# Performance work log

Hardware: AMD Instinct MI355X
Metric: run time of the kernel (lower is better)

The kernel has to match this reference:

```python
import jax, jax.numpy as jnp
import numpy as np

DIM = 512; HEADS = 8; DH = 64; M = 256; ITERS = 6; N_PATCH = 10000; N_CLASSES = 2


def layernorm(x, w, b, eps=1e-5):
    mu = x.mean(-1, keepdims=True)
    var = ((x - mu) ** 2).mean(-1, keepdims=True)
    return (x - mu) * jax.lax.rsqrt(var + eps) * w + b


def pinv_iter(x, iters=ITERS):
    # Moore-Penrose iterative pseudo-inverse (lucidrains nystrom-attention)
    abs_x = jnp.abs(x)
    col = abs_x.sum(-1)
    row = abs_x.sum(-2)
    z = jnp.swapaxes(x, -1, -2) / (jnp.max(col) * jnp.max(row))
    I = jnp.eye(x.shape[-1], dtype=x.dtype)
    for _ in range(iters):
        xz = x @ z
        z = 0.25 * z @ (13 * I - xz @ (15 * I - xz @ (7 * I - xz)))
    return z


def nystrom_attn(x, qkv_w, out_w, out_b, res_w):
    b, n, _ = x.shape
    pad = (-n) % M  # front-pad so n divisible by num_landmarks
    xp = jnp.pad(x, ((0, 0), (pad, 0), (0, 0)))
    npad = n + pad
    qkv = (xp @ qkv_w).reshape(b, npad, 3, HEADS, DH)
    q = jnp.transpose(qkv[:, :, 0], (0, 2, 1, 3)) * (DH ** -0.5)  # [b,h,n,d]
    k = jnp.transpose(qkv[:, :, 1], (0, 2, 1, 3))
    v = jnp.transpose(qkv[:, :, 2], (0, 2, 1, 3))
    l = npad // M
    q_l = q.reshape(b, HEADS, M, l, DH).mean(3)  # landmark means [b,h,m,d]
    k_l = k.reshape(b, HEADS, M, l, DH).mean(3)
    attn1 = jax.nn.softmax(jnp.einsum('bhnd,bhmd->bhnm', q, k_l), -1)
    attn2 = jax.nn.softmax(jnp.einsum('bhid,bhjd->bhij', q_l, k_l), -1)
    attn3 = jax.nn.softmax(jnp.einsum('bhmd,bhnd->bhmn', q_l, k), -1)
    out = (attn1 @ pinv_iter(attn2)) @ (attn3 @ v)  # [b,h,n,d]
    pk = (res_w.shape[2] - 1) // 2
    out = out + jax.lax.conv_general_dilated(
        v, res_w, (1, 1), [(pk, pk), (0, 0)], feature_group_count=HEADS)
    out = jnp.transpose(out, (0, 2, 1, 3)).reshape(b, npad, HEADS * DH)
    out = out @ out_w + out_b
    return out[:, -n:]


def ppeg(x, H, W, w7, b7, w5, b5, w3, b3):
    B, _, C = x.shape
    cls_tok, feat = x[:, :1], x[:, 1:]
    f = jnp.transpose(feat, (0, 2, 1)).reshape(B, C, H, W)
    def dw(w, b):
        p = w.shape[2] // 2
        return jax.lax.conv_general_dilated(
            f, w, (1, 1), [(p, p), (p, p)], feature_group_count=C) + b[None, :, None, None]
    y = f + dw(w7, b7) + dw(w5, b5) + dw(w3, b3)
    y = jnp.transpose(y.reshape(B, C, H * W), (0, 2, 1))
    return jnp.concatenate([cls_tok, y], axis=1)


def setup_inputs() -> dict:
    key = jax.random.key(0)
    ks = jax.random.split(key, 16)
    d = {
        'x': jax.random.normal(ks[0], (1, N_PATCH, DIM), jnp.float32),
        'cls_token': jax.random.normal(ks[1], (1, 1, DIM), jnp.float32) * 1e-6,
        'ln1_w': jnp.ones((DIM,), jnp.float32), 'ln1_b': jnp.zeros((DIM,), jnp.float32),
        'qkv1_w': jax.random.normal(ks[2], (DIM, 3 * DIM), jnp.float32) * 0.03,
        'out1_w': jax.random.normal(ks[3], (DIM, DIM), jnp.float32) * 0.04,
        'out1_b': jnp.zeros((DIM,), jnp.float32),
        'res1_w': jax.random.normal(ks[4], (HEADS, 1, 33, 1), jnp.float32) * 0.1,
        'p7_w': jax.random.normal(ks[5], (DIM, 1, 7, 7), jnp.float32) * 0.1,
        'p7_b': jnp.zeros((DIM,), jnp.float32),
        'p5_w': jax.random.normal(ks[6], (DIM, 1, 5, 5), jnp.float32) * 0.1,
        'p5_b': jnp.zeros((DIM,), jnp.float32),
        'p3_w': jax.random.normal(ks[7], (DIM, 1, 3, 3), jnp.float32) * 0.1,
        'p3_b': jnp.zeros((DIM,), jnp.float32),
        'ln2_w': jnp.ones((DIM,), jnp.float32), 'ln2_b': jnp.zeros((DIM,), jnp.float32),
        'qkv2_w': jax.random.normal(ks[8], (DIM, 3 * DIM), jnp.float32) * 0.03,
        'out2_w': jax.random.normal(ks[9], (DIM, DIM), jnp.float32) * 0.04,
        'out2_b': jnp.zeros((DIM,), jnp.float32),
        'res2_w': jax.random.normal(ks[10], (HEADS, 1, 33, 1), jnp.float32) * 0.1,
        'norm_w': jnp.ones((DIM,), jnp.float32), 'norm_b': jnp.zeros((DIM,), jnp.float32),
        'fc2_w': jax.random.normal(ks[11], (DIM, N_CLASSES), jnp.float32) * 0.06,
        'fc2_b': jnp.zeros((N_CLASSES,), jnp.float32),
        'pc_w': jax.random.normal(ks[12], (DIM, N_CLASSES), jnp.float32) * 0.06,
        'pc_b': jnp.zeros((N_CLASSES,), jnp.float32),
    }
    return d


def reference(x, cls_token, ln1_w, ln1_b, qkv1_w, out1_w, out1_b, res1_w,
              p7_w, p7_b, p5_w, p5_b, p3_w, p3_b,
              ln2_w, ln2_b, qkv2_w, out2_w, out2_b, res2_w,
              norm_w, norm_b, fc2_w, fc2_b, pc_w, pc_b):
    h = x.astype(jnp.float32)
    B, n0, C = h.shape
    _H = int(np.ceil(np.sqrt(n0))); _W = _H
    add = _H * _W - n0
    if add > 0:
        h = jnp.concatenate([h, h[:, :add]], axis=1)
    h = jnp.concatenate([jnp.broadcast_to(cls_token, (B, 1, C)), h], axis=1)
    h = h + nystrom_attn(layernorm(h, ln1_w, ln1_b), qkv1_w, out1_w, out1_b, res1_w)
    h = ppeg(h, _H, _W, p7_w, p7_b, p5_w, p5_b, p3_w, p3_b)
    h = h + nystrom_attn(layernorm(h, ln2_w, ln2_b), qkv2_w, out2_w, out2_b, res2_w)
    hn = layernorm(h, norm_w, norm_b)
    cls_f = hn[:, 0]
    patch_f = hn[:, 1:]
    if add > 0:
        patch_f = patch_f[:, :n0]
    bag_logits = cls_f @ fc2_w + fc2_b
    patch_logits = patch_f @ pc_w + pc_b
    patch_scores = jax.nn.softmax(patch_logits, -1)
    return bag_logits, patch_logits, patch_scores
```

## Files before the change

### kernel.cpp

```cpp
#include <hip/hip_runtime.h>
#include <hip/hip_bf16.h>

#define DIM    512
#define HEADS  8
#define DHD    64
#define MLAND  256
#define NTOK   10001
#define NPATCH 10000
#define NPAD   10240
#define PADR   239
#define LFAC   40
#define MOUT   10112
#define NSPLIT 8

typedef __bf16 bf16x8_t __attribute__((ext_vector_type(8)));
typedef float  f32x4_t  __attribute__((ext_vector_type(4)));
typedef short  short8_t __attribute__((ext_vector_type(8)));

__device__ inline bf16x8_t bzero8() {
    union { short8_t s; bf16x8_t b; } u;
    u.s = (short8_t){0, 0, 0, 0, 0, 0, 0, 0};
    return u.b;
}

#define GLDS(gp, lp) __builtin_amdgcn_global_load_lds( \
    (const __attribute__((address_space(1))) void*)(gp), \
    (__attribute__((address_space(3))) void*)(lp), 16, 0, 0)

__global__ void k_concat(const float* __restrict__ x, const float* __restrict__ cls,
                         float* __restrict__ h) {
    int idx = blockIdx.x * 256 + threadIdx.x;
    if (idx >= NTOK * DIM) return;
    int row = idx / DIM, col = idx % DIM;
    h[idx] = (row == 0) ? cls[col] : x[(row - 1) * DIM + col];
}

__global__ void k_layernorm_bf(const float* __restrict__ h, const float* __restrict__ w,
                               const float* __restrict__ b, __hip_bfloat16* __restrict__ xbf) {
    int row = blockIdx.x;
    const float* r = h + (long)row * DIM;
    int t = threadIdx.x;
    float v0 = r[t], v1 = r[t + 256];
    __shared__ float red[256];
    red[t] = v0 + v1; __syncthreads();
    for (int o = 128; o > 0; o >>= 1) { if (t < o) red[t] += red[t + o]; __syncthreads(); }
    float mu = red[0] * (1.f / DIM); __syncthreads();
    float d0 = v0 - mu, d1 = v1 - mu;
    red[t] = d0 * d0 + d1 * d1; __syncthreads();
    for (int o = 128; o > 0; o >>= 1) { if (t < o) red[t] += red[t + o]; __syncthreads(); }
    float rstd = rsqrtf(red[0] * (1.f / DIM) + 1e-5f);
    long base = (long)(PADR + row) * DIM;
    xbf[base + t]       = __float2bfloat16(d0 * rstd * w[t] + b[t]);
    xbf[base + t + 256] = __float2bfloat16(d1 * rstd * w[t + 256] + b[t + 256]);
}

__global__ void k_zerobf(__hip_bfloat16* __restrict__ p, int n) {
    int i = blockIdx.x * 256 + threadIdx.x;
    if (i < n) p[i] = __float2bfloat16(0.f);
}
__global__ void k_wt_cvt(const float* __restrict__ W, __hip_bfloat16* __restrict__ Wt,
                         int K, int N) {
    __shared__ float tile[32][33];
    int k0 = blockIdx.x * 32, n0 = blockIdx.y * 32;
    int lx = threadIdx.x % 32, ly = threadIdx.x / 32;
    for (int i = 0; i < 32; i += 8) tile[ly + i][lx] = W[(long)(k0 + ly + i) * N + n0 + lx];
    __syncthreads();
    for (int i = 0; i < 32; i += 8)
        Wt[(long)(n0 + ly + i) * K + k0 + lx] = __float2bfloat16(tile[lx][ly + i]);
}
__global__ void k_vt(const __hip_bfloat16* __restrict__ vh, __hip_bfloat16* __restrict__ vt) {
    __shared__ __hip_bfloat16 tile[32][33];
    int n0 = blockIdx.x * 32, d0 = blockIdx.y * 32, h = blockIdx.z;
    int lx = threadIdx.x % 32, ly = threadIdx.x / 32;
    for (int i = 0; i < 32; i += 8)
        tile[ly + i][lx] = vh[((long)h * NPAD + n0 + ly + i) * 64 + d0 + lx];
    __syncthreads();
    for (int i = 0; i < 32; i += 8)
        vt[((long)h * 64 + d0 + ly + i) * NPAD + n0 + lx] = tile[lx][ly + i];
}

__global__ __launch_bounds__(256) void k_qkv_gemm(
    const __hip_bfloat16* __restrict__ A, const __hip_bfloat16* __restrict__ Bt,
    __hip_bfloat16* __restrict__ qh, __hip_bfloat16* __restrict__ kh,
    __hip_bfloat16* __restrict__ vh)
{
    const int K = 512;
    __shared__ unsigned short As[128 * 64];
    __shared__ unsigned short Bs[128 * 64];
    int tid = threadIdx.x;
    int m0 = blockIdx.y * 128, n0 = blockIdx.x * 128;
    int wave = tid >> 6, lane = tid & 63;
    int wm = (wave & 1) * 64, wn = (wave >> 1) * 64;
    f32x4_t zero4 = {0.f, 0.f, 0.f, 0.f};
    f32x4_t acc[4][4];
#pragma unroll
    for (int i = 0; i < 4; i++)
#pragma unroll
        for (int j = 0; j < 4; j++) acc[i][j] = zero4;
    int quad = lane >> 4, fr = lane & 15;
    int lrow8 = lane >> 3, gls = lane & 7;
    int gg = gls ^ lrow8;

    for (int k0 = 0; k0 < K; k0 += 64) {
        __syncthreads();
#pragma unroll
        for (int rnd = 0; rnd < 4; rnd++) {
            int r0 = rnd * 32 + wave * 8;
            int ar = r0 + lrow8;
            GLDS(A  + (long)(m0 + ar) * K + k0 + gg * 8, &As[r0 * 64]);
            GLDS(Bt + (long)(n0 + ar) * K + k0 + gg * 8, &Bs[r0 * 64]);
        }
        __syncthreads();
#pragma unroll
        for (int ks = 0; ks < 2; ks++) {
            int sg = (ks * 4 + quad) ^ (fr & 7);
            bf16x8_t af[4], bq[4];
#pragma unroll
            for (int i = 0; i < 4; i++) {
                af[i] = *(const bf16x8_t*)&As[(wm + i * 16 + fr) * 64 + sg * 8];
                bq[i] = *(const bf16x8_t*)&Bs[(wn + i * 16 + fr) * 64 + sg * 8];
            }
#pragma unroll
            for (int i = 0; i < 4; i++)
#pragma unroll
                for (int j = 0; j < 4; j++)
                    acc[i][j] = __builtin_amdgcn_mfma_f32_16x16x32_bf16(af[i], bq[j], acc[i][j], 0, 0, 0);
        }
    }
    int col = lane & 15, rq = lane >> 4;
#pragma unroll
    for (int j = 0; j < 4; j++) {
        int c = n0 + wn + j * 16 + col;
        int sect = c >> 9;
        int hh = (c >> 6) & 7;
        int d = c & 63;
        __hip_bfloat16* dst = (sect == 0) ? qh : (sect == 1) ? kh : vh;
        float sc = (sect == 0) ? 0.125f : 1.f;
#pragma unroll
        for (int i = 0; i < 4; i++) {
            int rbase = m0 + wm + i * 16 + rq * 4;
#pragma unroll
            for (int rr = 0; rr < 4; rr++) {
                int r = rbase + rr;
                dst[((long)hh * NPAD + r) * 64 + d] = __float2bfloat16(acc[i][j][rr] * sc);
            }
        }
    }
}

__global__ __launch_bounds__(256) void k_mfma_gemm(
    const __hip_bfloat16* __restrict__ A, const __hip_bfloat16* __restrict__ Bt,
    float* __restrict__ C, int M, int N, int K, int Mstore,
    const float* __restrict__ bias, int accum)
{
    __shared__ unsigned short As[128 * 64];
    __shared__ unsigned short Bs[128 * 64];
    int tid = threadIdx.x;
    int m0 = blockIdx.y * 128, n0 = blockIdx.x * 128;
    int wave = tid >> 6, lane = tid & 63;
    int wm = (wave & 1) * 64, wn = (wave >> 1) * 64;
    f32x4_t zero4 = {0.f, 0.f, 0.f, 0.f};
    f32x4_t acc[4][4];
#pragma unroll
    for (int i = 0; i < 4; i++)
#pragma unroll
        for (int j = 0; j < 4; j++) acc[i][j] = zero4;
    int quad = lane >> 4, fr = lane & 15;
    int lrow8 = lane >> 3, gls = lane & 7;
    int gg = gls ^ lrow8;

    for (int k0 = 0; k0 < K; k0 += 64) {
        __syncthreads();
#pragma unroll
        for (int rnd = 0; rnd < 4; rnd++) {
            int r0 = rnd * 32 + wave * 8;
            int ar = r0 + lrow8;
            GLDS(A  + (long)(m0 + ar) * K + k0 + gg * 8, &As[r0 * 64]);
            GLDS(Bt + (long)(n0 + ar) * K + k0 + gg * 8, &Bs[r0 * 64]);
        }
        __syncthreads();
#pragma unroll
        for (int ks = 0; ks < 2; ks++) {
            int sg = (ks * 4 + quad) ^ (fr & 7);
            bf16x8_t af[4], bq[4];
#pragma unroll
            for (int i = 0; i < 4; i++) {
                af[i] = *(const bf16x8_t*)&As[(wm + i * 16 + fr) * 64 + sg * 8];
                bq[i] = *(const bf16x8_t*)&Bs[(wn + i * 16 + fr) * 64 + sg * 8];
            }
#pragma unroll
            for (int i = 0; i < 4; i++)
#pragma unroll
                for (int j = 0; j < 4; j++)
                    acc[i][j] = __builtin_amdgcn_mfma_f32_16x16x32_bf16(af[i], bq[j], acc[i][j], 0, 0, 0);
        }
    }
    int col = lane & 15, rq = lane >> 4;
#pragma unroll
    for (int j = 0; j < 4; j++) {
        int c = n0 + wn + j * 16 + col;
        float bsv = bias ? bias[c] : 0.f;
#pragma unroll
        for (int i = 0; i < 4; i++) {
            int rbase = m0 + wm + i * 16 + rq * 4;
#pragma unroll
            for (int rr = 0; rr < 4; rr++) {
                int r = rbase + rr;
                if (r >= Mstore) continue;
                float v = acc[i][j][rr] + bsv;
                long off = (long)r * N + c;
                if (accum) C[off] += v; else C[off] = v;
            }
        }
    }
}

__global__ __launch_bounds__(256) void k_mfma_t64(
    const __hip_bfloat16* __restrict__ A, long lda, long abatch, int arowmax,
    const __hip_bfloat16* __restrict__ Bt, long ldb, long bbatch,
    __hip_bfloat16* __restrict__ Cbf, long ldc, long cbatch, int ksplit)
{
    int h = blockIdx.z;
    const __hip_bfloat16* Ab = A + (long)h * abatch;
    const __hip_bfloat16* Bb = Bt + (long)h * bbatch;
    int m0 = blockIdx.y * 128;
    int kbeg = blockIdx.x * ksplit, kend = kbeg + ksplit;
    int wave = threadIdx.x >> 6, lane = threadIdx.x & 63;
    int wm = (wave & 1) * 64, wn = (wave >> 1) * 32;
    int fr = lane & 15, quad = lane >> 4;
    f32x4_t zero4 = {0.f, 0.f, 0.f, 0.f};
    f32x4_t acc[4][2];
#pragma unroll
    for (int i = 0; i < 4; i++) { acc[i][0] = zero4; acc[i][1] = zero4; }
    for (int k0 = kbeg; k0 < kend; k0 += 32) {
        bf16x8_t bq[2];
#pragma unroll
        for (int j = 0; j < 2; j++)
            bq[j] = *(const bf16x8_t*)(Bb + (long)(wn + j * 16 + fr) * ldb + k0 + quad * 8);
#pragma unroll
        for (int i = 0; i < 4; i++) {
            int r = m0 + wm + i * 16 + fr;
            bf16x8_t af = (r < arowmax) ? *(const bf16x8_t*)(Ab + (long)r * lda + k0 + quad * 8)
                                        : bzero8();
#pragma unroll
            for (int j = 0; j < 2; j++)
                acc[i][j] = __builtin_amdgcn_mfma_f32_16x16x32_bf16(af, bq[j], acc[i][j], 0, 0, 0);
        }
    }
#pragma unroll
    for (int i = 0; i < 4; i++)
#pragma unroll
        for (int j = 0; j < 2; j++)
#pragma unroll
            for (int rr = 0; rr < 4; rr++) {
                int r = m0 + wm + i * 16 + quad * 4 + rr;
                int c = wn + j * 16 + fr;
                Cbf[(long)h * cbatch + (long)c * ldc + r] = __float2bfloat16(acc[i][j][rr]);
            }
}

__global__ __launch_bounds__(256) void k_mm256(
    const __hip_bfloat16* __restrict__ Aa, const __hip_bfloat16* __restrict__ Bt,
    float s, float acoef, const __hip_bfloat16* __restrict__ Aadd,
    __hip_bfloat16* __restrict__ Ca, __hip_bfloat16* __restrict__ Ct)
{
    int hd = blockIdx.z;
    long hb = (long)hd * 65536;
    int m0 = blockIdx.y * 64, n0 = blockIdx.x * 32;
    int wave = threadIdx.x >> 6, lane = threadIdx.x & 63;
    int fr = lane & 15, quad = lane >> 4;
    int mrow = m0 + wave * 16;
    f32x4_t zero4 = {0.f, 0.f, 0.f, 0.f};
    f32x4_t acc[2];
    acc[0] = zero4; acc[1] = zero4;
#pragma unroll
    for (int k0 = 0; k0 < 256; k0 += 32) {
        bf16x8_t af = *(const bf16x8_t*)(Aa + hb + (long)(mrow + fr) * 256 + k0 + quad * 8);
#pragma unroll
        for (int j = 0; j < 2; j++) {
            bf16x8_t bq = *(const bf16x8_t*)(Bt + hb + (long)(n0 + j * 16 + fr) * 256 + k0 + quad * 8);
            acc[j] = __builtin_amdgcn_mfma_f32_16x16x32_bf16(af, bq, acc[j], 0, 0, 0);
        }
    }
#pragma unroll
    for (int j = 0; j < 2; j++)
#pragma unroll
        for (int rr = 0; rr < 4; rr++) {
            int r = mrow + quad * 4 + rr;
            int c = n0 + j * 16 + fr;
            float v = s * acc[j][rr];
            if (Aadd) v += acoef * __bfloat162float(Aadd[hb + (long)r * 256 + c]);
            __hip_bfloat16 bv = __float2bfloat16(v);
            if (Ca) Ca[hb + (long)r * 256 + c] = bv;
            if (Ct) Ct[hb + (long)c * 256 + r] = bv;
        }
}

__global__ __launch_bounds__(256) void k_attn3f(
    const __hip_bfloat16* __restrict__ qlbf, const __hip_bfloat16* __restrict__ kh,
    const __hip_bfloat16* __restrict__ vt, float* __restrict__ part)
{
    int ns = blockIdx.x, mt = blockIdx.y, h = blockIdx.z;
    int wave = threadIdx.x >> 6, lane = threadIdx.x & 63;
    int fr = lane & 15, quad = lane >> 4;
    int lrow8 = lane >> 3, gls = lane & 7;
    int gg = gls ^ lrow8;
    int vsub = lane >> 5, vgrp = lane & 31;
    int swz = fr & 7;
    __shared__ unsigned short Ks[2][256 * 64];
    __shared__ unsigned short Vs[2][64 * 256];
    __shared__ __hip_bfloat16 Pl[64 * 136];
    f32x4_t zero4 = {0.f, 0.f, 0.f, 0.f};
    bf16x8_t aq[2];
    {
        const __hip_bfloat16* qb = qlbf + (long)h * 16384 + (long)(mt * 64 + wave * 16 + fr) * 64;
        aq[0] = *(const bf16x8_t*)(qb + quad * 8);
        aq[1] = *(const bf16x8_t*)(qb + 32 + quad * 8);
    }
    f32x4_t O[4];
#pragma unroll
    for (int j = 0; j < 4; j++) O[j] = zero4;
    float mr[4] = {-1e30f, -1e30f, -1e30f, -1e30f};
    float lr[4] = {0.f, 0.f, 0.f, 0.f};
    const __hip_bfloat16* kb = kh + (long)h * NPAD * 64;
    const __hip_bfloat16* vb = vt + (long)h * 64 * NPAD;

#define STAGE_KV(N0, KD, VD) do { \
    _Pragma("unroll") \
    for (int rnd = 0; rnd < 8; rnd++) { \
        int r0 = rnd * 32 + wave * 8; \
        GLDS(kb + (long)((N0) + r0 + lrow8) * 64 + gg * 8, (KD) + r0 * 64); \
    } \
    _Pragma("unroll") \
    for (int rnd = 0; rnd < 8; rnd++) { \
        int v0 = rnd * 8 + wave * 2; \
        int vrow = v0 + vsub; \
        GLDS(vb + (long)vrow * NPAD + (N0) + (vgrp ^ (vrow & 7)) * 8, (VD) + v0 * 256); \
    } \
} while (0)

    STAGE_KV(ns * 1280, &Ks[0][0], &Vs[0][0]);

    for (int nt = 0; nt < 5; nt++) {
        int bsel = nt & 1;
        if (nt < 4) {
            int n1 = ns * 1280 + (nt + 1) * 256;
            STAGE_KV(n1, &Ks[bsel ^ 1][0], &Vs[bsel ^ 1][0]);
            asm volatile("s_waitcnt vmcnt(16)" ::: "memory");
        } else {
            asm volatile("s_waitcnt vmcnt(0)" ::: "memory");
        }
        __builtin_amdgcn_s_barrier();

        const unsigned short* Kc = &Ks[bsel][0];
        const unsigned short* Vc = &Vs[bsel][0];
        f32x4_t s[16];
#pragma unroll
        for (int j = 0; j < 16; j++) s[j] = zero4;
#pragma unroll
        for (int j = 0; j < 16; j++) {
            const unsigned short* kr = Kc + (j * 16 + fr) * 64;
            bf16x8_t b0 = *(const bf16x8_t*)(kr + (quad ^ swz) * 8);
            bf16x8_t b1 = *(const bf16x8_t*)(kr + ((quad ^ swz) ^ 4) * 8);
            s[j] = __builtin_amdgcn_mfma_f32_16x16x32_bf16(aq[0], b0, s[j], 0, 0, 0);
            s[j] = __builtin_amdgcn_mfma_f32_16x16x32_bf16(aq[1], b1, s[j], 0, 0, 0);
        }
        float tm[4] = {-1e30f, -1e30f, -1e30f, -1e30f};
#pragma unroll
        for (int j = 0; j < 16; j++)
#pragma unroll
            for (int rr = 0; rr < 4; rr++) tm[rr] = fmaxf(tm[rr], s[j][rr]);
#pragma unroll
        for (int rr = 0; rr < 4; rr++) {
#pragma unroll
            for (int o = 8; o > 0; o >>= 1) tm[rr] = fmaxf(tm[rr], __shfl_xor(tm[rr], o));
        }
        float alpha[4], ts[4];
#pragma unroll
        for (int rr = 0; rr < 4; rr++) {
            float mnew = fmaxf(mr[rr], tm[rr]);
            alpha[rr] = __expf(mr[rr] - mnew);
            mr[rr] = mnew;
            ts[rr] = 0.f;
        }
#pragma unroll
        for (int j = 0; j < 16; j++)
#pragma unroll
            for (int rr = 0; rr < 4; rr++) {
                float e = __expf(s[j][rr] - mr[rr]);
                s[j][rr] = e;
                ts[rr] += e;
            }
#pragma unroll
        for (int rr = 0; rr < 4; rr++) {
#pragma unroll
            for (int o = 8; o > 0; o >>= 1) ts[rr] += __shfl_xor(ts[rr], o);
            lr[rr] = lr[rr] * alpha[rr] + ts[rr];
        }
#pragma unroll
        for (int j = 0; j < 4; j++)
#pragma unroll
            for (int rr = 0; rr < 4; rr++) O[j][rr] *= alpha[rr];
#pragma unroll
        for (int half = 0; half < 2; half++) {
#pragma unroll
            for (int j = 0; j < 8; j++)
#pragma unroll
                for (int rr = 0; rr < 4; rr++)
                    Pl[(wave * 16 + quad * 4 + rr) * 136 + j * 16 + fr] =
                        __float2bfloat16(s[half * 8 + j][rr]);
#pragma unroll
            for (int k0 = 0; k0 < 128; k0 += 32) {
                bf16x8_t af = *(const bf16x8_t*)&Pl[(wave * 16 + fr) * 136 + k0 + quad * 8];
                int gb = (half * 128 + k0) >> 3;
#pragma unroll
                for (int j = 0; j < 4; j++) {
                    const unsigned short* vr = Vc + (j * 16 + fr) * 256;
                    bf16x8_t bq = *(const bf16x8_t*)(vr + ((gb + quad) ^ swz) * 8);
                    O[j] = __builtin_amdgcn_mfma_f32_16x16x32_bf16(af, bq, O[j], 0, 0, 0);
                }
            }
        }
        asm volatile("" ::: "memory");
        __builtin_amdgcn_s_barrier();
    }
#undef STAGE_KV

    float* Ob = part + (long)((h * 4 + mt) * NSPLIT + ns) * 4224;
#pragma unroll
    for (int j = 0; j < 4; j++)
#pragma unroll
        for (int rr = 0; rr < 4; rr++)
            Ob[(wave * 16 + quad * 4 + rr) * 64 + j * 16 + fr] = O[j][rr];
    if (fr == 0) {
#pragma unroll
        for (int rr = 0; rr < 4; rr++) {
            Ob[4096 + wave * 16 + quad * 4 + rr] = mr[rr];
            Ob[4160 + wave * 16 + quad * 4 + rr] = lr[rr];
        }
    }
}

__global__ void k_a3comb(const float* __restrict__ part, __hip_bfloat16* __restrict__ a3vt) {
    int mt = blockIdx.x, h = blockIdx.y, t = threadIdx.x;
    int row = t >> 2, c0 = (t & 3) * 16;
    long base = (long)((h * 4 + mt) * NSPLIT) * 4224;
    float M = -1e30f;
    for (int s = 0; s < NSPLIT; s++) M = fmaxf(M, part[base + s * 4224 + 4096 + row]);
    float L = 0.f;
    float o[16];
#pragma unroll
    for (int c = 0; c < 16; c++) o[c] = 0.f;
    for (int s = 0; s < NSPLIT; s++) {
        const float* pb = part + base + (long)s * 4224;
        float w = __expf(pb[4096 + row] - M);
        L += pb[4160 + row] * w;
#pragma unroll
        for (int c = 0; c < 16; c++) o[c] += w * pb[row * 64 + c0 + c];
    }
    float invL = 1.f / L;
#pragma unroll
    for (int c = 0; c < 16; c++)
        a3vt[(long)h * 16384 + (long)(c0 + c) * 256 + mt * 64 + row] = __float2bfloat16(o[c] * invL);
}

__global__ void k_conv_res(const __hip_bfloat16* __restrict__ vh, const float* __restrict__ resw,
                           __hip_bfloat16* __restrict__ convbf) {
    int e4 = blockIdx.x * 256 + threadIdx.x;
    if (e4 >= NTOK * 128) return;
    int i = e4 >> 7;
    int c4 = (e4 & 127) * 4;
    int hh = c4 >> 6, d = c4 & 63;
    int n = PADR + i;
    const __hip_bfloat16* vb = vh + (long)hh * NPAD * 64 + d;
    float a0 = 0.f, a1 = 0.f, a2 = 0.f, a3 = 0.f;
#pragma unroll
    for (int t = 0; t < 33; t++) {
        int nn = n - 16 + t;
        if (nn < NPAD) {
            float w = resw[hh * 33 + t];
            uint2 pv = *(const uint2*)(vb + (long)nn * 64);
            __hip_bfloat16 vv[4];
            *(uint2*)vv = pv;
            a0 += w * __bfloat162float(vv[0]);
            a1 += w * __bfloat162float(vv[1]);
            a2 += w * __bfloat162float(vv[2]);
            a3 += w * __bfloat162float(vv[3]);
        }
    }
    __hip_bfloat16 o[4] = {__float2bfloat16(a0), __float2bfloat16(a1),
                           __float2bfloat16(a2), __float2bfloat16(a3)};
    *(uint2*)(convbf + (long)i * DIM + c4) = *(uint2*)o;
}

__global__ __launch_bounds__(256, 4) void k_attn1f(
    const __hip_bfloat16* __restrict__ qh, const __hip_bfloat16* __restrict__ klbf,
    const __hip_bfloat16* __restrict__ w2bt, const __hip_bfloat16* __restrict__ convbf,
    __hip_bfloat16* __restrict__ abf)
{
    int h = blockIdx.y;
    int i0 = blockIdx.x * 32;
    __shared__ __hip_bfloat16 Pl[64 * 136];
    __shared__ float mS[2][2][16];
    int tid = threadIdx.x;
    int wave = tid >> 6, lane = tid & 63;
    int rg = wave & 1, lh = wave >> 1;
    int fr = lane & 15, quad = lane >> 4;
    const __hip_bfloat16* kb = klbf + (long)h * (MLAND * DHD) + (long)lh * 128 * DHD;
    f32x4_t zero4 = {0.f, 0.f, 0.f, 0.f};

    float cp[4][4];
    if (lh == 0) {
#pragma unroll
        for (int j = 0; j < 4; j++)
#pragma unroll
            for (int rr = 0; rr < 4; rr++) {
                int r = i0 + rg * 16 + quad * 4 + rr;
                cp[j][rr] = (r < NTOK)
                    ? __bfloat162float(convbf[(long)r * DIM + h * DHD + j * 16 + fr]) : 0.f;
            }
    }

    f32x4_t s[8];
#pragma unroll
    for (int j = 0; j < 8; j++) s[j] = zero4;
    int arow = i0 + rg * 16 + fr;
    const __hip_bfloat16* qrow = qh + ((long)h * NPAD + PADR + arow) * 64;
#pragma unroll
    for (int k0 = 0; k0 < 64; k0 += 32) {
        bf16x8_t af = (arow < NTOK) ? *(const bf16x8_t*)(qrow + k0 + quad * 8) : bzero8();
#pragma unroll
        for (int j = 0; j < 8; j++) {
            bf16x8_t bq = *(const bf16x8_t*)(kb + (long)(j * 16 + fr) * DHD + k0 + quad * 8);
            s[j] = __builtin_amdgcn_mfma_f32_16x16x32_bf16(af, bq, s[j], 0, 0, 0);
        }
    }
    float sum[4] = {0.f, 0.f, 0.f, 0.f};
#pragma unroll
    for (int j = 0; j < 8; j++)
#pragma unroll
        for (int rr = 0; rr < 4; rr++) {
            float e = __expf(s[j][rr]);
            s[j][rr] = e;
            sum[rr] += e;
        }
#pragma unroll
    for (int rr = 0; rr < 4; rr++) {
#pragma unroll
        for (int o = 8; o > 0; o >>= 1) sum[rr] += __shfl_xor(sum[rr], o);
    }
    if (fr == 0) {
#pragma unroll
        for (int rr = 0; rr < 4; rr++) mS[lh][rg][quad * 4 + rr] = sum[rr];
    }
#pragma unroll
    for (int j = 0; j < 8; j++)
#pragma unroll
        for (int rr = 0; rr < 4; rr++)
            Pl[(wave * 16 + quad * 4 + rr) * 136 + j * 16 + fr] = __float2bfloat16(s[j][rr]);
    __syncthreads();
    float fac[4];
#pragma unroll
    for (int rr = 0; rr < 4; rr++)
        fac[rr] = 1.f / (sum[rr] + mS[lh ^ 1][rg][quad * 4 + rr]);
    const __hip_bfloat16* wb = w2bt + (long)h * (DHD * MLAND) + lh * 128;
    f32x4_t oc[4];
#pragma unroll
    for (int j = 0; j < 4; j++) oc[j] = zero4;
#pragma unroll
    for (int k0 = 0; k0 < 128; k0 += 32) {
        bf16x8_t af = *(const bf16x8_t*)&Pl[(wave * 16 + fr) * 136 + k0 + quad * 8];
#pragma unroll
        for (int j = 0; j < 4; j++) {
            bf16x8_t bq = *(const bf16x8_t*)(wb + (long)(j * 16 + fr) * MLAND + k0 + quad * 8);
            oc[j] = __builtin_amdgcn_mfma_f32_16x16x32_bf16(af, bq, oc[j], 0, 0, 0);
        }
    }
#pragma unroll
    for (int j = 0; j < 4; j++)
#pragma unroll
        for (int rr = 0; rr < 4; rr++) oc[j][rr] *= fac[rr];
    __syncthreads();
    float* ex = (float*)Pl;
    if (lh == 1) {
#pragma unroll
        for (int j = 0; j < 4; j++)
#pragma unroll
            for (int rr = 0; rr < 4; rr++)
                ex[(rg * 16 + quad * 4 + rr) * 64 + j * 16 + fr] = oc[j][rr];
    }
    __syncthreads();
    if (lh == 0) {
#pragma unroll
        for (int j = 0; j < 4; j++)
#pragma unroll
            for (int rr = 0; rr < 4; rr++) {
                int r = i0 + rg * 16 + quad * 4 + rr;
                if (r < NTOK) {
                    float v = oc[j][rr] + ex[(rg * 16 + quad * 4 + rr) * 64 + j * 16 + fr]
                              + cp[j][rr];
                    abf[(long)r * DIM + h * DHD + j * 16 + fr] = __float2bfloat16(v);
                }
            }
    }
}

__global__ void k_landmarks(const __hip_bfloat16* __restrict__ qh,
                            const __hip_bfloat16* __restrict__ kh,
                            float* __restrict__ ql, float* __restrict__ kl,
                            __hip_bfloat16* __restrict__ qlbf, __hip_bfloat16* __restrict__ klbf) {
    int m = blockIdx.x, h = blockIdx.y, d = threadIdx.x;
    float sq = 0.f, sk = 0.f;
    for (int j = 0; j < LFAC; j++) {
        long base = ((long)h * NPAD + m * LFAC + j) * 64 + d;
        sq += __bfloat162float(qh[base]);
        sk += __bfloat162float(kh[base]);
    }
    long o = ((long)h * MLAND + m) * DHD + d;
    float vq = sq * (1.f / LFAC), vk = sk * (1.f / LFAC);
    ql[o] = vq; kl[o] = vk;
    qlbf[o] = __float2bfloat16(vq);
    klbf[o] = __float2bfloat16(vk);
}

__global__ void k_attn2(const float* __restrict__ ql, const float* __restrict__ kl,
                        float* __restrict__ attn2, __hip_bfloat16* __restrict__ attn2bf) {
    int i = blockIdx.x, h = blockIdx.y, j = threadIdx.x;
    __shared__ float q[64];
    __shared__ float red[256];
    if (j < 64) q[j] = ql[((long)h * MLAND + i) * DHD + j];
    __syncthreads();
    const float* kr = kl + ((long)h * MLAND + j) * DHD;
    float s = 0.f;
#pragma unroll 8
    for (int d = 0; d < 64; d++) s += q[d] * kr[d];
    red[j] = s; __syncthreads();
    for (int o = 128; o > 0; o >>= 1) { if (j < o) red[j] = fmaxf(red[j], red[j + o]); __syncthreads(); }
    float mx = red[0]; __syncthreads();
    float e = __expf(s - mx);
    red[j] = e; __syncthreads();
    for (int o = 128; o > 0; o >>= 1) { if (j < o) red[j] += red[j + o]; __syncthreads(); }
    float v = e / red[0];
    long off = ((long)h * MLAND + i) * MLAND + j;
    attn2[off] = v;
    attn2bf[off] = __float2bfloat16(v);
}

__global__ void k_colrow(const float* __restrict__ x, float* __restrict__ scal) {
    int h = blockIdx.x, t = threadIdx.x;
    const float* xh = x + (long)h * MLAND * MLAND;
    float cs = 0.f, rs = 0.f;
    for (int j = 0; j < MLAND; j++) {
        cs += fabsf(xh[(long)t * MLAND + j]);
        rs += fabsf(xh[(long)j * MLAND + t]);
    }
    __shared__ float red[256];
    red[t] = cs; __syncthreads();
    for (int o = 128; o > 0; o >>= 1) { if (t < o) red[t] = fmaxf(red[t], red[t + o]); __syncthreads(); }
    if (t == 0) scal[2 + h] = red[0];
    __syncthreads();
    red[t] = rs; __syncthreads();
    for (int o = 128; o > 0; o >>= 1) { if (t < o) red[t] = fmaxf(red[t], red[t + o]); __syncthreads(); }
    if (t == 0) scal[10 + h] = red[0];
}

__global__ void k_tscale2(const float* __restrict__ x, const float* __restrict__ scal,
                          __hip_bfloat16* __restrict__ za, __hip_bfloat16* __restrict__ zt) {
    int h = blockIdx.z;
    int tj = blockIdx.x * 32, ti = blockIdx.y * 32;
    __shared__ float tile[32][33];
    const float* xh = x + (long)h * 65536;
    int lx = threadIdx.x % 32, ly = threadIdx.x / 32;
    float cm = scal[2], rm = scal[10];
#pragma unroll
    for (int k = 1; k < 8; k++) {
        cm = fmaxf(cm, scal[2 + k]);
        rm = fmaxf(rm, scal[10 + k]);
    }
    float inv = 1.f / (cm * rm);
    for (int yy = 0; yy < 32; yy += 8) {
        float v = xh[(long)(ti + ly + yy) * MLAND + tj + lx];
        tile[ly + yy][lx] = v;
        zt[(long)h * 65536 + (long)(ti + ly + yy) * MLAND + tj + lx] = __float2bfloat16(v * inv);
    }
    __syncthreads();
    for (int yy = 0; yy < 32; yy += 8)
        za[(long)h * 65536 + (long)(tj + ly + yy) * MLAND + ti + lx] =
            __float2bfloat16(tile[lx][ly + yy] * inv);
}

__global__ void k_tfwd(const float* __restrict__ h, float* __restrict__ ft) {
    __shared__ float tile[32][33];
    int t0 = blockIdx.x * 32, c0 = blockIdx.y * 32;
    int lx = threadIdx.x % 32, ly = threadIdx.x / 32;
    for (int i = 0; i < 32; i += 8) {
        int t = t0 + ly + i;
        if (t < NPATCH) tile[ly + i][lx] = h[(long)(1 + t) * DIM + c0 + lx];
    }
    __syncthreads();
    for (int i = 0; i < 32; i += 8) {
        int c = c0 + ly + i, t = t0 + lx;
        if (t < NPATCH) ft[(long)c * NPATCH + t] = tile[lx][ly + i];
    }
}

__global__ __launch_bounds__(256) void k_ppeg2(
    const float* __restrict__ ft, float* __restrict__ yt,
    const float* __restrict__ w7, const float* __restrict__ b7,
    const float* __restrict__ w5, const float* __restrict__ b5,
    const float* __restrict__ w3, const float* __restrict__ b3)
{
    int s = blockIdx.x, c = blockIdx.y;
    __shared__ float tile[26][106];
    __shared__ float wt[49];
    int tid = threadIdx.x;
    int r0 = s * 20 - 3;
    for (int idx = tid; idx < 26 * 106; idx += 256) {
        int rr = idx / 106, cc = idx % 106;
        int gy = r0 + rr, gx = cc - 3;
        float v = 0.f;
        if (gy >= 0 && gy < 100 && gx >= 0 && gx < 100)
            v = ft[(long)c * NPATCH + gy * 100 + gx];
        tile[rr][cc] = v;
    }
    if (tid < 49) {
        int dy = tid / 7 - 3, dx = tid % 7 - 3;
        float w = w7[c * 49 + tid];
        if (dy >= -2 && dy <= 2 && dx >= -2 && dx <= 2) w += w5[c * 25 + (dy + 2) * 5 + (dx + 2)];
        if (dy >= -1 && dy <= 1 && dx >= -1 && dx <= 1) w += w3[c * 9 + (dy + 1) * 3 + (dx + 1)];
        wt[tid] = w;
    }
    __syncthreads();
    float bsum = b7[c] + b5[c] + b3[c];
    for (int p = tid; p < 2000; p += 256) {
        int ly = p / 100, lx = p % 100;
        float acc = tile[ly + 3][lx + 3] + bsum;
#pragma unroll
        for (int dy = 0; dy < 7; dy++)
#pragma unroll
            for (int dx = 0; dx < 7; dx++)
                acc += wt[dy * 7 + dx] * tile[ly + dy][lx + dx];
        yt[(long)c * NPATCH + (s * 20 + ly) * 100 + lx] = acc;
    }
}

__global__ void k_tback(const float* __restrict__ yt, float* __restrict__ h) {
    __shared__ float tile[32][33];
    int t0 = blockIdx.x * 32, c0 = blockIdx.y * 32;
    int lx = threadIdx.x % 32, ly = threadIdx.x / 32;
    for (int i = 0; i < 32; i += 8) {
        int c = c0 + ly + i, t = t0 + lx;
        if (t < NPATCH) tile[ly + i][lx] = yt[(long)c * NPATCH + t];
    }
    __syncthreads();
    for (int i = 0; i < 32; i += 8) {
        int t = t0 + ly + i;
        if (t < NPATCH) h[(long)(1 + t) * DIM + c0 + lx] = tile[lx][ly + i];
    }
}

__global__ void k_final(const float* __restrict__ h, const float* __restrict__ nw,
                        const float* __restrict__ nb,
                        const float* __restrict__ fc2w, const float* __restrict__ fc2b,
                        const float* __restrict__ pcw, const float* __restrict__ pcb,
                        float* __restrict__ out)
{
    int row = blockIdx.x;
    int t = threadIdx.x;
    const float* r = h + (long)row * DIM;
    float v0 = r[t], v1 = r[t + 256];
    __shared__ float red[256];
    red[t] = v0 + v1; __syncthreads();
    for (int o = 128; o > 0; o >>= 1) { if (t < o) red[t] += red[t + o]; __syncthreads(); }
    float mu = red[0] * (1.f / DIM); __syncthreads();
    float d0 = v0 - mu, d1 = v1 - mu;
    red[t] = d0 * d0 + d1 * d1; __syncthreads();
    for (int o = 128; o > 0; o >>= 1) { if (t < o) red[t] += red[t + o]; __syncthreads(); }
    float rstd = rsqrtf(red[0] * (1.f / DIM) + 1e-5f); __syncthreads();
    float h0 = d0 * rstd * nw[t] + nb[t];
    float h1 = d1 * rstd * nw[t + 256] + nb[t + 256];
    const float* w = (row == 0) ? fc2w : pcw;
    float p0 = h0 * w[t * 2] + h1 * w[(t + 256) * 2];
    float p1 = h0 * w[t * 2 + 1] + h1 * w[(t + 256) * 2 + 1];
    red[t] = p0; __syncthreads();
    for (int o = 128; o > 0; o >>= 1) { if (t < o) red[t] += red[t + o]; __syncthreads(); }
    float l0 = red[0]; __syncthreads();
    red[t] = p1; __syncthreads();
    for (int o = 128; o > 0; o >>= 1) { if (t < o) red[t] += red[t + o]; __syncthreads(); }
    if (t == 0) {
        float l1 = red[0];
        const float* bb = (row == 0) ? fc2b : pcb;
        float a0 = l0 + bb[0], a1 = l1 + bb[1];
        if (row == 0) { out[0] = a0; out[1] = a1; }
        else {
            long i = row - 1;
            out[2 + i * 2] = a0;
            out[2 + i * 2 + 1] = a1;
            float m = fmaxf(a0, a1);
            float e0 = __expf(a0 - m), e1 = __expf(a1 - m);
            float inv = 1.f / (e0 + e1);
            out[2 + 2 * NPATCH + i * 2] = e0 * inv;
            out[2 + 2 * NPATCH + i * 2 + 1] = e1 * inv;
        }
    }
}

extern "C" void kernel_launch(void* const* d_in, const int* in_sizes, int n_in,
                              void* d_out, int out_size, void* d_ws, size_t ws_size,
                              hipStream_t stream)
{
    const float* x     = (const float*)d_in[0];
    const float* cls   = (const float*)d_in[1];
    const float* ln1w  = (const float*)d_in[2];
    const float* ln1b  = (const float*)d_in[3];
    const float* qkv1w = (const float*)d_in[4];
    const float* out1w = (const float*)d_in[5];
    const float* out1b = (const float*)d_in[6];
    const float* res1w = (const float*)d_in[7];
    const float* p7w   = (const float*)d_in[8];
    const float* p7b   = (const float*)d_in[9];
    const float* p5w   = (const float*)d_in[10];
    const float* p5b   = (const float*)d_in[11];
    const float* p3w   = (const float*)d_in[12];
    const float* p3b   = (const float*)d_in[13];
    const float* ln2w  = (const float*)d_in[14];
    const float* ln2b  = (const float*)d_in[15];
    const float* qkv2w = (const float*)d_in[16];
    const float* out2w = (const float*)d_in[17];
    const float* out2b = (const float*)d_in[18];
    const float* res2w = (const float*)d_in[19];
    const float* normw = (const float*)d_in[20];
    const float* normb = (const float*)d_in[21];
    const float* fc2w  = (const float*)d_in[22];
    const float* fc2b  = (const float*)d_in[23];
    const float* pcw   = (const float*)d_in[24];
    const float* pcb   = (const float*)d_in[25];
    float* out = (float*)d_out;

    float* p = (float*)d_ws;
    float* h      = p; p += 5120512;
    float* yt     = p; p += 5120512;
    float* ql     = p; p += 131072;
    float* kl     = p; p += 131072;
    float* x2     = p; p += 524288;
    float* scal   = p; p += 32;
    float* part   = p; p += 1081344;
    float* ft     = p; p += 5120512;
    __hip_bfloat16* qh     = (__hip_bfloat16*)p; p += 2621440;
    __hip_bfloat16* kh     = (__hip_bfloat16*)p; p += 2621440;
    __hip_bfloat16* vh     = (__hip_bfloat16*)p; p += 2621440;
    __hip_bfloat16* xbf    = (__hip_bfloat16*)p; p += 2621440;
    __hip_bfloat16* abf    = (__hip_bfloat16*)p; p += 2588672;
    __hip_bfloat16* convbf = (__hip_bfloat16*)p; p += 2560256;
    __hip_bfloat16* qw1t   = (__hip_bfloat16*)p; p += 393216;
    __hip_bfloat16* qw2t   = (__hip_bfloat16*)p; p += 393216;
    __hip_bfloat16* ow1t   = (__hip_bfloat16*)p; p += 131072;
    __hip_bfloat16* ow2t   = (__hip_bfloat16*)p; p += 131072;
    __hip_bfloat16* x2a    = (__hip_bfloat16*)p; p += 262144;
    __hip_bfloat16* za     = (__hip_bfloat16*)p; p += 262144;
    __hip_bfloat16* zt     = (__hip_bfloat16*)p; p += 262144;
    __hip_bfloat16* za2    = (__hip_bfloat16*)p; p += 262144;
    __hip_bfloat16* zt2    = (__hip_bfloat16*)p; p += 262144;
    __hip_bfloat16* xza    = (__hip_bfloat16*)p; p += 262144;
    __hip_bfloat16* xzt    = (__hip_bfloat16*)p; p += 262144;
    __hip_bfloat16* t1t    = (__hip_bfloat16*)p; p += 262144;
    __hip_bfloat16* t2t    = (__hip_bfloat16*)p; p += 262144;
    __hip_bfloat16* qlbf   = (__hip_bfloat16*)p; p += 65536;
    __hip_bfloat16* klbf   = (__hip_bfloat16*)p; p += 65536;
    __hip_bfloat16* vt     = (__hip_bfloat16*)p; p += 2621440;
    __hip_bfloat16* a3vt   = (__hip_bfloat16*)p; p += 65536;
    __hip_bfloat16* w2bt   = (__hip_bfloat16*)p; p += 65536;

    k_concat<<<dim3((NTOK * DIM + 255) / 256), 256, 0, stream>>>(x, cls, h);
    k_wt_cvt<<<dim3(16, 48), 256, 0, stream>>>(qkv1w, qw1t, 512, 1536);
    k_wt_cvt<<<dim3(16, 48), 256, 0, stream>>>(qkv2w, qw2t, 512, 1536);
    k_wt_cvt<<<dim3(16, 16), 256, 0, stream>>>(out1w, ow1t, 512, 512);
    k_wt_cvt<<<dim3(16, 16), 256, 0, stream>>>(out2w, ow2t, 512, 512);
    k_zerobf<<<dim3((PADR * DIM + 255) / 256), 256, 0, stream>>>(xbf, PADR * DIM);

    auto layer = [&](const float* lnw, const float* lnb, const __hip_bfloat16* qwt,
                     const __hip_bfloat16* owt, const float* outb, const float* resw) {
        k_layernorm_bf<<<NTOK, 256, 0, stream>>>(h, lnw, lnb, xbf);
        k_qkv_gemm<<<dim3(12, 80), 256, 0, stream>>>(xbf, qwt, qh, kh, vh);
        k_vt<<<dim3(320, 2, HEADS), 256, 0, stream>>>(vh, vt);
        k_landmarks<<<dim3(MLAND, HEADS), 64, 0, stream>>>(qh, kh, ql, kl, qlbf, klbf);
        k_attn2<<<dim3(MLAND, HEADS), 256, 0, stream>>>(ql, kl, x2, x2a);
        k_colrow<<<HEADS, 256, 0, stream>>>(x2, scal);
        k_tscale2<<<dim3(8, 8, HEADS), 256, 0, stream>>>(x2, scal, za, zt);
        {
            __hip_bfloat16 *zra = za, *zrt = zt, *zoa = za2, *zot = zt2;
            dim3 g(8, 4, HEADS);
            for (int it = 0; it < 6; it++) {
                k_mm256<<<g, 256, 0, stream>>>(x2a, zrt, 1.f, 0.f, nullptr, xza, xzt);
                k_mm256<<<g, 256, 0, stream>>>(xza, xzt, -1.f, 7.f, xza, nullptr, t1t);
                k_mm256<<<g, 256, 0, stream>>>(xza, t1t, -1.f, 15.f, xza, nullptr, t2t);
                k_mm256<<<g, 256, 0, stream>>>(zra, t2t, -0.25f, 3.25f, zra, zoa, zot);
                __hip_bfloat16* tmp;
                tmp = zra; zra = zoa; zoa = tmp;
                tmp = zrt; zrt = zot; zot = tmp;
            }
        }
        k_attn3f<<<dim3(NSPLIT, 4, HEADS), 256, 0, stream>>>(qlbf, kh, vt, part);
        k_a3comb<<<dim3(4, HEADS), 256, 0, stream>>>(part, a3vt);
        k_mfma_t64<<<dim3(1, 2, HEADS), 256, 0, stream>>>(
            za, 256, 65536, 256, a3vt, 256, 16384,
            w2bt, 256, 16384, 256);
        k_conv_res<<<dim3((NTOK * 128 + 255) / 256), 256, 0, stream>>>(vh, resw, convbf);
        k_attn1f<<<dim3(313, HEADS), 256, 0, stream>>>(qh, klbf, w2bt, convbf, abf);
        k_mfma_gemm<<<dim3(4, 79), 256, 0, stream>>>(abf, owt, h, MOUT, 512, 512,
                                                     NTOK, outb, 1);
    };

    layer(ln1w, ln1b, qw1t, ow1t, out1b, res1w);

    k_tfwd<<<dim3(313, 16), 256, 0, stream>>>(h, ft);
    k_ppeg2<<<dim3(5, 512), 256, 0, stream>>>(ft, yt, p7w, p7b, p5w, p5b, p3w, p3b);
    k_tback<<<dim3(313, 16), 256, 0, stream>>>(yt, h);

    layer(ln2w, ln2b, qw2t, ow2t, out2b, res2w);

    k_final<<<NTOK, 256, 0, stream>>>(h, normw, normb, fc2w, fc2b, pcw, pcb, out);
    (void)in_sizes; (void)n_in; (void)out_size; (void)ws_size;
}
```

Measured before the change: 981.6 us.

## Double-buffer LDS in GEMM kernels and widen attn1 tiles to 64 rows

After: 965.8 us. About the same (-1.6%).

```diff
diff --git a/kernel.cpp b/kernel.cpp
--- a/kernel.cpp
+++ b/kernel.cpp
@@ -85,8 +85,8 @@
     __hip_bfloat16* __restrict__ vh)
 {
     const int K = 512;
-    __shared__ unsigned short As[128 * 64];
-    __shared__ unsigned short Bs[128 * 64];
+    __shared__ unsigned short As[2][128 * 64];
+    __shared__ unsigned short Bs[2][128 * 64];
     int tid = threadIdx.x;
     int m0 = blockIdx.y * 128, n0 = blockIdx.x * 128;
     int wave = tid >> 6, lane = tid & 63;
@@ -101,24 +101,34 @@
     int lrow8 = lane >> 3, gls = lane & 7;
     int gg = gls ^ lrow8;
 
+#define STAGE_AB(K0, AD, BD) do { \
+    _Pragma("unroll") \
+    for (int rnd = 0; rnd < 4; rnd++) { \
+        int r0 = rnd * 32 + wave * 8; \
+        int ar = r0 + lrow8; \
+        GLDS(A  + (long)(m0 + ar) * K + (K0) + gg * 8, (AD) + r0 * 64); \
+        GLDS(Bt + (long)(n0 + ar) * K + (K0) + gg * 8, (BD) + r0 * 64); \
+    } \
+} while (0)
+
+    STAGE_AB(0, &As[0][0], &Bs[0][0]);
     for (int k0 = 0; k0 < K; k0 += 64) {
-        __syncthreads();
-#pragma unroll
-        for (int rnd = 0; rnd < 4; rnd++) {
-            int r0 = rnd * 32 + wave * 8;
-            int ar = r0 + lrow8;
-            GLDS(A  + (long)(m0 + ar) * K + k0 + gg * 8, &As[r0 * 64]);
-            GLDS(Bt + (long)(n0 + ar) * K + k0 + gg * 8, &Bs[r0 * 64]);
-        }
-        __syncthreads();
+        int b = (k0 >> 6) & 1;
+        if (k0 + 64 < K) {
+            STAGE_AB(k0 + 64, &As[b ^ 1][0], &Bs[b ^ 1][0]);
+            asm volatile("s_waitcnt vmcnt(8)" ::: "memory");
+        } else {
+            asm volatile("s_waitcnt vmcnt(0)" ::: "memory");
+        }
+        __builtin_amdgcn_s_barrier();
 #pragma unroll
         for (int ks = 0; ks < 2; ks++) {
             int sg = (ks * 4 + quad) ^ (fr & 7);
             bf16x8_t af[4], bq[4];
 #pragma unroll
             for (int i = 0; i < 4; i++) {
-                af[i] = *(const bf16x8_t*)&As[(wm + i * 16 + fr) * 64 + sg * 8];
-                bq[i] = *(const bf16x8_t*)&Bs[(wn + i * 16 + fr) * 64 + sg * 8];
+                af[i] = *(const bf16x8_t*)&As[b][(wm + i * 16 + fr) * 64 + sg * 8];
+                bq[i] = *(const bf16x8_t*)&Bs[b][(wn + i * 16 + fr) * 64 + sg * 8];
             }
 #pragma unroll
             for (int i = 0; i < 4; i++)
@@ -126,7 +136,10 @@
                 for (int j = 0; j < 4; j++)
                     acc[i][j] = __builtin_amdgcn_mfma_f32_16x16x32_bf16(af[i], bq[j], acc[i][j], 0, 0, 0);
         }
-    }
+        asm volatile("" ::: "memory");
+        __builtin_amdgcn_s_barrier();
+    }
+#undef STAGE_AB
     int col = lane & 15, rq = lane >> 4;
 #pragma unroll
     for (int j = 0; j < 4; j++) {
@@ -153,8 +166,8 @@
     float* __restrict__ C, int M, int N, int K, int Mstore,
     const float* __restrict__ bias, int accum)
 {
-    __shared__ unsigned short As[128 * 64];
-    __shared__ unsigned short Bs[128 * 64];
+    __shared__ unsigned short As[2][128 * 64];
+    __shared__ unsigned short Bs[2][128 * 64];
     int tid = threadIdx.x;
     int m0 = blockIdx.y * 128, n0 = blockIdx.x * 128;
     int wave = tid >> 6, lane = tid & 63;
@@ -169,24 +182,34 @@
     int lrow8 = lane >> 3, gls = lane & 7;
     int gg = gls ^ lrow8;
 
+#define STAGE_AB(K0, AD, BD) do { \
+    _Pragma("unroll") \
+    for (int rnd = 0; rnd < 4; rnd++) { \
+        int r0 = rnd * 32 + wave * 8; \
+        int ar = r0 + lrow8; \
+        GLDS(A  + (long)(m0 + ar) * K + (K0) + gg * 8, (AD) + r0 * 64); \
+        GLDS(Bt + (long)(n0 + ar) * K + (K0) + gg * 8, (BD) + r0 * 64); \
+    } \
+} while (0)
+
+    STAGE_AB(0, &As[0][0], &Bs[0][0]);
     for (int k0 = 0; k0 < K; k0 += 64) {
-        __syncthreads();
-#pragma unroll
-        for (int rnd = 0; rnd < 4; rnd++) {
-            int r0 = rnd * 32 + wave * 8;
-            int ar = r0 + lrow8;
-            GLDS(A  + (long)(m0 + ar) * K + k0 + gg * 8, &As[r0 * 64]);
-            GLDS(Bt + (long)(n0 + ar) * K + k0 + gg * 8, &Bs[r0 * 64]);
-        }
-        __syncthreads();
+        int b = (k0 >> 6) & 1;
+        if (k0 + 64 < K) {
+            STAGE_AB(k0 + 64, &As[b ^ 1][0], &Bs[b ^ 1][0]);
+            asm volatile("s_waitcnt vmcnt(8)" ::: "memory");
+        } else {
+            asm volatile("s_waitcnt vmcnt(0)" ::: "memory");
+        }
+        __builtin_amdgcn_s_barrier();
 #pragma unroll
         for (int ks = 0; ks < 2; ks++) {
             int sg = (ks * 4 + quad) ^ (fr & 7);
             bf16x8_t af[4], bq[4];
 #pragma unroll
             for (int i = 0; i < 4; i++) {
-                af[i] = *(const bf16x8_t*)&As[(wm + i * 16 + fr) * 64 + sg * 8];
-                bq[i] = *(const bf16x8_t*)&Bs[(wn + i * 16 + fr) * 64 + sg * 8];
+                af[i] = *(const bf16x8_t*)&As[b][(wm + i * 16 + fr) * 64 + sg * 8];
+                bq[i] = *(const bf16x8_t*)&Bs[b][(wn + i * 16 + fr) * 64 + sg * 8];
             }
 #pragma unroll
             for (int i = 0; i < 4; i++)
@@ -194,7 +217,10 @@
                 for (int j = 0; j < 4; j++)
                     acc[i][j] = __builtin_amdgcn_mfma_f32_16x16x32_bf16(af[i], bq[j], acc[i][j], 0, 0, 0);
         }
-    }
+        asm volatile("" ::: "memory");
+        __builtin_amdgcn_s_barrier();
+    }
+#undef STAGE_AB
     int col = lane & 15, rq = lane >> 4;
 #pragma unroll
     for (int j = 0; j < 4; j++) {
@@ -493,15 +519,15 @@
     *(uint2*)(convbf + (long)i * DIM + c4) = *(uint2*)o;
 }
 
-__global__ __launch_bounds__(256, 4) void k_attn1f(
+__global__ __launch_bounds__(256, 3) void k_attn1f(
     const __hip_bfloat16* __restrict__ qh, const __hip_bfloat16* __restrict__ klbf,
     const __hip_bfloat16* __restrict__ w2bt, const __hip_bfloat16* __restrict__ convbf,
     __hip_bfloat16* __restrict__ abf)
 {
     int h = blockIdx.y;
-    int i0 = blockIdx.x * 32;
+    int i0 = blockIdx.x * 64;
     __shared__ __hip_bfloat16 Pl[64 * 136];
-    __shared__ float mS[2][2][16];
+    __shared__ float mS[2][2][2][16];
     int tid = threadIdx.x;
     int wave = tid >> 6, lane = tid & 63;
     int rg = wave & 1, lh = wave >> 1;
@@ -509,85 +535,105 @@
     const __hip_bfloat16* kb = klbf + (long)h * (MLAND * DHD) + (long)lh * 128 * DHD;
     f32x4_t zero4 = {0.f, 0.f, 0.f, 0.f};
 
-    float cp[4][4];
-    if (lh == 0) {
-#pragma unroll
-        for (int j = 0; j < 4; j++)
-#pragma unroll
-            for (int rr = 0; rr < 4; rr++) {
-                int r = i0 + rg * 16 + quad * 4 + rr;
-                cp[j][rr] = (r < NTOK)
-                    ? __bfloat162float(convbf[(long)r * DIM + h * DHD + j * 16 + fr]) : 0.f;
-            }
-    }
-
-    f32x4_t s[8];
-#pragma unroll
-    for (int j = 0; j < 8; j++) s[j] = zero4;
-    int arow = i0 + rg * 16 + fr;
-    const __hip_bfloat16* qrow = qh + ((long)h * NPAD + PADR + arow) * 64;
+    f32x4_t s0[8], s1[8];
+#pragma unroll
+    for (int j = 0; j < 8; j++) { s0[j] = zero4; s1[j] = zero4; }
+    int arow0 = i0 + rg * 16 + fr;
+    int arow1 = arow0 + 32;
+    const __hip_bfloat16* qrow = qh + ((long)h * NPAD + PADR + arow0) * 64;
 #pragma unroll
     for (int k0 = 0; k0 < 64; k0 += 32) {
-        bf16x8_t af = (arow < NTOK) ? *(const bf16x8_t*)(qrow + k0 + quad * 8) : bzero8();
+        bf16x8_t af0 = (arow0 < NTOK) ? *(const bf16x8_t*)(qrow + k0 + quad * 8) : bzero8();
+        bf16x8_t af1 = (arow1 < NTOK) ? *(const bf16x8_t*)(qrow + 32 * 64 + k0 + quad * 8) : bzero8();
 #pragma unroll
         for (int j = 0; j < 8; j++) {
             bf16x8_t bq = *(const bf16x8_t*)(kb + (long)(j * 16 + fr) * DHD + k0 + quad * 8);
-            s[j] = __builtin_amdgcn_mfma_f32_16x16x32_bf16(af, bq, s[j], 0, 0, 0);
-        }
-    }
-    float sum[4] = {0.f, 0.f, 0.f, 0.f};
+            s0[j] = __builtin_amdgcn_mfma_f32_16x16x32_bf16(af0, bq, s0[j], 0, 0, 0);
+            s1[j] = __builtin_amdgcn_mfma_f32_16x16x32_bf16(af1, bq, s1[j], 0, 0, 0);
+        }
+    }
+    float sum0[4] = {0.f, 0.f, 0.f, 0.f}, sum1[4] = {0.f, 0.f, 0.f, 0.f};
 #pragma unroll
     for (int j = 0; j < 8; j++)
 #pragma unroll
         for (int rr = 0; rr < 4; rr++) {
-            float e = __expf(s[j][rr]);
-            s[j][rr] = e;
-            sum[rr] += e;
+            float e0 = __expf(s0[j][rr]); s0[j][rr] = e0; sum0[rr] += e0;
+            float e1 = __expf(s1[j][rr]); s1[j][rr] = e1; sum1[rr] += e1;
         }
 #pragma unroll
     for (int rr = 0; rr < 4; rr++) {
 #pragma unroll
-        for (int o = 8; o > 0; o >>= 1) sum[rr] += __shfl_xor(sum[rr], o);
+        for (int o = 8; o > 0; o >>= 1) {
+            sum0[rr] += __shfl_xor(sum0[rr], o);
+            sum1[rr] += __shfl_xor(sum1[rr], o);
+        }
     }
     if (fr == 0) {
 #pragma unroll
-        for (int rr = 0; rr < 4; rr++) mS[lh][rg][quad * 4 + rr] = sum[rr];
+        for (int rr = 0; rr < 4; rr++) {
+            mS[0][lh][rg][quad * 4 + rr] = sum0[rr];
+            mS[1][lh][rg][quad * 4 + rr] = sum1[rr];
+        }
     }
 #pragma unroll
     for (int j = 0; j < 8; j++)
 #pragma unroll
-        for (int rr = 0; rr < 4; rr++)
-            Pl[(wave * 16 + quad * 4 + rr) * 136 + j * 16 + fr] = __float2bfloat16(s[j][rr]);
-    __syncthreads();
-    float fac[4];
-#pragma unroll
-    for (int rr = 0; rr < 4; rr++)
-        fac[rr] = 1.f / (sum[rr] + mS[lh ^ 1][rg][quad * 4 + rr]);
+        for (int rr = 0; rr < 4; rr++) {
+            Pl[(rg * 16 + quad * 4 + rr) * 136 + j * 16 + fr]      = __float2bfloat16(s0[j][rr]);
+            Pl[(32 + rg * 16 + quad * 4 + rr) * 136 + j * 16 + fr] = __float2bfloat16(s1[j][rr]);
+        }
+    __syncthreads();
+    float fac0[4], fac1[4];
+#pragma unroll
+    for (int rr = 0; rr < 4; rr++) {
+        fac0[rr] = 1.f / (sum0[rr] + mS[0][lh ^ 1][rg][quad * 4 + rr]);
+        fac1[rr] = 1.f / (sum1[rr] + mS[1][lh ^ 1][rg][quad * 4 + rr]);
+    }
+    float cp[2][4][4];
+    if (lh == 0) {
+#pragma unroll
+        for (int rt = 0; rt < 2; rt++)
+#pragma unroll
+            for (int j = 0; j < 4; j++)
+#pragma unroll
+                for (int rr = 0; rr < 4; rr++) {
+                    int r = i0 + rt * 32 + rg * 16 + quad * 4 + rr;
+                    cp[rt][j][rr] = (r < NTOK)
+                        ? __bfloat162float(convbf[(long)r * DIM + h * DHD + j * 16 + fr]) : 0.f;
+                }
+    }
     const __hip_bfloat16* wb = w2bt + (long)h * (DHD * MLAND) + lh * 128;
-    f32x4_t oc[4];
-#pragma unroll
-    for (int j = 0; j < 4; j++) oc[j] = zero4;
+    f32x4_t oc0[4], oc1[4];
+#pragma unroll
+    for (int j = 0; j < 4; j++) { oc0[j] = zero4; oc1[j] = zero4; }
 #pragma unroll
     for (int k0 = 0; k0 < 128; k0 += 32) {
-        bf16x8_t af = *(const bf16x8_t*)&Pl[(wave * 16 + fr) * 136 + k0 + quad * 8];
+        bf16x8_t af0 = *(const bf16x8_t*)&Pl[(rg * 16 + fr) * 136 + k0 + quad * 8];
+        bf16x8_t af1 = *(const bf16x8_t*)&Pl[(32 + rg * 16 + fr) * 136 + k0 + quad * 8];
 #pragma unroll
         for (int j = 0; j < 4; j++) {
             bf16x8_t bq = *(const bf16x8_t*)(wb + (long)(j * 16 + fr) * MLAND + k0 + quad * 8);
-            oc[j] = __builtin_amdgcn_mfma_f32_16x16x32_bf16(af, bq, oc[j], 0, 0, 0);
+            oc0[j] = __builtin_amdgcn_mfma_f32_16x16x32_bf16(af0, bq, oc0[j], 0, 0, 0);
+            oc1[j] = __builtin_amdgcn_mfma_f32_16x16x32_bf16(af1, bq, oc1[j], 0, 0, 0);
         }
     }
 #pragma unroll
     for (int j = 0; j < 4; j++)
 #pragma unroll
-        for (int rr = 0; rr < 4; rr++) oc[j][rr] *= fac[rr];
+        for (int rr = 0; rr < 4; rr++) {
+            oc0[j][rr] *= fac0[rr];
+            oc1[j][rr] *= fac1[rr];
+        }
     __syncthreads();
     float* ex = (float*)Pl;
     if (lh == 1) {
 #pragma unroll
         for (int j = 0; j < 4; j++)
 #pragma unroll
-            for (int rr = 0; rr < 4; rr++)
-                ex[(rg * 16 + quad * 4 + rr) * 64 + j * 16 + fr] = oc[j][rr];
+            for (int rr = 0; rr < 4; rr++) {
+                ex[(rg * 16 + quad * 4 + rr) * 64 + j * 16 + fr]      = oc0[j][rr];
+                ex[(32 + rg * 16 + quad * 4 + rr) * 64 + j * 16 + fr] = oc1[j][rr];
+            }
     }
     __syncthreads();
     if (lh == 0) {
@@ -595,11 +641,16 @@
         for (int j = 0; j < 4; j++)
 #pragma unroll
             for (int rr = 0; rr < 4; rr++) {
-                int r = i0 + rg * 16 + quad * 4 + rr;
-                if (r < NTOK) {
-                    float v = oc[j][rr] + ex[(rg * 16 + quad * 4 + rr) * 64 + j * 16 + fr]
-                              + cp[j][rr];
-                    abf[(long)r * DIM + h * DHD + j * 16 + fr] = __float2bfloat16(v);
+                int lr0 = rg * 16 + quad * 4 + rr;
+                int r0 = i0 + lr0;
+                if (r0 < NTOK) {
+                    float v = oc0[j][rr] + ex[lr0 * 64 + j * 16 + fr] + cp[0][j][rr];
+                    abf[(long)r0 * DIM + h * DHD + j * 16 + fr] = __float2bfloat16(v);
+                }
+                int r1 = r0 + 32;
+                if (r1 < NTOK) {
+                    float v = oc1[j][rr] + ex[(32 + lr0) * 64 + j * 16 + fr] + cp[1][j][rr];
+                    abf[(long)r1 * DIM + h * DHD + j * 16 + fr] = __float2bfloat16(v);
                 }
             }
     }
@@ -906,7 +957,7 @@
             za, 256, 65536, 256, a3vt, 256, 16384,
             w2bt, 256, 16384, 256);
         k_conv_res<<<dim3((NTOK * 128 + 255) / 256), 256, 0, stream>>>(vh, resw, convbf);
-        k_attn1f<<<dim3(313, HEADS), 256, 0, stream>>>(qh, klbf, w2bt, convbf, abf);
+        k_attn1f<<<dim3(157, HEADS), 256, 0, stream>>>(qh, klbf, w2bt, convbf, abf);
         k_mfma_gemm<<<dim3(4, 79), 256, 0, stream>>>(abf, owt, h, MOUT, 512, 512,
                                                      NTOK, outb, 1);
     };
```
